# Performance work log

Measured on AMD Instinct MI355X. Metric: run time of the kernel, lower is better.

## Reference

```python
import math
from itertools import combinations
import jax, jax.numpy as jnp
import numpy as np

B, N, KR, KA, T = 16, 96, 16, 8, 4
RCR, RCA = 5.2, 3.5


def setup_inputs() -> dict:
    key = jax.random.key(0)
    k1, k2 = jax.random.split(key)
    coords = jax.random.normal(k1, (B, N, 3), dtype=jnp.float32) * 3.0
    atom_types = jax.random.randint(k2, (N,), 0, T)
    EtaR = jnp.full((T, KR), 16.0, dtype=jnp.float32)
    ShfR = jnp.tile(jnp.linspace(0.9, 5.0, KR, dtype=jnp.float32), (T, 1))
    Zeta = jnp.full((T, KA), 32.0, dtype=jnp.float32)
    EtaA = jnp.tile(jnp.linspace(0.5, 8.0, KA, dtype=jnp.float32), (T, 1))
    return {"coords": coords, "atom_types": atom_types,
            "EtaR": EtaR, "ShfR": ShfR, "Zeta": Zeta, "EtaA": EtaA}


def _pairwise_vector(coords):
    # coords: [B, N, 3] -> rij: [B, N, N-1, 3] (diagonal removed, same order as masked_select)
    n = coords.shape[1]
    idx = np.array([[j for j in range(n) if j != i] for i in range(n)])  # [N, N-1]
    rij = coords[:, :, None, :] - coords[:, None, :, :]                   # [B, N, N, 3]
    return rij[:, np.arange(n)[:, None], idx]                             # [B, N, N-1, 3]


def reference(coords, atom_types, EtaR, ShfR, Zeta, EtaA):
    rij = _pairwise_vector(coords)                 # [B, N, N-1, 3]
    er = EtaR[atom_types]                          # [N, KR]
    sr = ShfR[atom_types]                          # [N, KR]
    ze = Zeta[atom_types]                          # [N, KA]
    ea = EtaA[atom_types]                          # [N, KA]

    # ---- G2 (radial) ----
    dij = jnp.linalg.norm(rij, axis=3)             # [B, N, N-1]
    fij = (jnp.cos(dij / RCR * math.pi) + 1) * 0.5
    g2 = jnp.sum(jnp.exp(-er[:, None, :] * (dij[..., None] - sr[:, None, :]) ** 2)
                 * fij[..., None], axis=2)         # [B, N, KR]

    # ---- G3 (angular) ----
    n1 = rij.shape[2]
    c = np.array(list(combinations(range(n1), 2)))  # [P, 2]
    rp = rij[:, :, c]                               # [B, N, P, 2, 3]
    r12, r13 = rp[:, :, :, 0], rp[:, :, :, 1]
    r23 = r12 - r13
    d12 = jnp.linalg.norm(r12, axis=3)              # [B, N, P]
    d13 = jnp.linalg.norm(r13, axis=3)
    d23 = jnp.linalg.norm(r23, axis=3)
    f12 = (jnp.cos(d12 / RCA * math.pi) + 1) * 0.5
    f13 = (jnp.cos(d13 / RCA * math.pi) + 1) * 0.5
    f23 = (jnp.cos(d23 / RCA * math.pi) + 1) * 0.5
    cosine = jnp.einsum('bnpk,bnpk->bnp', r12, r13) / (d12 * d13)
    g3 = jnp.sum(2.0 ** (1 - ze[:, None, :])
                 * (1 + cosine[..., None]) ** ze[:, None, :]
                 * jnp.exp(-ea[:, None, :] * (d12 ** 2 + d13 ** 2 + d23 ** 2)[..., None])
                 * (f12 * f13 * f23)[..., None], axis=2)  # [B, N, KA]

    return jnp.concatenate((g2, g3), axis=2)        # [B, N, KR+KA]
```

## Files before the change

### kernel.cpp

```cpp
#include <hip/hip_runtime.h>

namespace {
constexpr int Bc  = 16;
constexpr int Nc  = 96;
constexpr int KRc = 16;
constexpr int KAc = 8;
constexpr int NOUT = KRc + KAc;
constexpr int NNb  = Nc - 1;
constexpr float RCRf = 5.2f;
constexpr float RCAf = 3.5f;
constexpr float L2E  = 1.4426950408889634f;
}

__device__ __forceinline__ float cos_rev(float rev) {
    return __builtin_amdgcn_cosf(__builtin_amdgcn_fractf(rev));
}
__device__ __forceinline__ float exp2g(float x) {
    return __builtin_amdgcn_exp2f(x);
}

__global__ __launch_bounds__(256, 6) void ani_feat_kernel(
    const float* __restrict__ coords,
    const int*   __restrict__ atom_types,
    const float* __restrict__ EtaR,
    const float* __restrict__ ShfR,
    const float* __restrict__ Zeta,
    const float* __restrict__ EtaA,
    float* __restrict__ out)
{
    const int bi = blockIdx.x;
    const int b  = bi / Nc;
    const int i  = bi - b * Nc;
    const int t  = threadIdx.x;
    const int lane = t & 63, wv = t >> 6;

    __shared__ float4 su[NNb];
    __shared__ float  ufa[NNb], sfr[NNb];
    __shared__ float4 ca4[NNb];
    __shared__ float  cfa[NNb], cfr[NNb];
    __shared__ float  pr[16][KRc];
    __shared__ float  red[4][KAc];
    __shared__ int    sM[2];

    const int ti = atom_types[i];

    bool fast;
    float ea0, dLs, c10, THR;
    {
        float z0 = Zeta[ti * KAc + 0];
        bool zu = true;
#pragma unroll
        for (int k = 1; k < KAc; ++k) zu = zu && (Zeta[ti * KAc + k] == z0);
        ea0 = EtaA[ti * KAc + 0] * L2E;
        float e1v = EtaA[ti * KAc + 1] * L2E;
        dLs = e1v - ea0;
        bool ar = true;
#pragma unroll
        for (int k = 2; k < KAc; ++k) {
            float ev = EtaA[ti * KAc + k] * L2E;
            ar = ar && (fabsf(ev - (ea0 + dLs * (float)k)) <=
                        1e-5f * fabsf(ev) + 1e-7f);
        }
        float eamin = fminf(ea0, ea0 + 7.0f * dLs);
        fast = zu && ar && (z0 == 32.0f) && (eamin > 1e-6f);
        THR  = fast ? (26.0f / eamin) : 1e30f;
        c10  = 1.0f - z0;
    }

    float st_ux = 0, st_uy = 0, st_uz = 0, st_d = 0, st_fa = 0, st_fr = 0;
    bool pred = false;
    if (t < NNb) {
        const float* cb = coords + (size_t)(b * Nc) * 3;
        int j = t + (t >= i);
        float dx = cb[i*3+0] - cb[j*3+0];
        float dy = cb[i*3+1] - cb[j*3+1];
        float dz = cb[i*3+2] - cb[j*3+2];
        float d2 = dx*dx + dy*dy + dz*dz;
        float d  = __builtin_amdgcn_sqrtf(d2);
        float inv = __builtin_amdgcn_rcpf(d);
        st_ux = dx*inv; st_uy = dy*inv; st_uz = dz*inv; st_d = d;
        st_fa = fmaf(cos_rev(d * (0.5f / RCAf)), 0.5f, 0.5f);
        st_fr = fmaf(cos_rev(d * (0.5f / RCRf)), 0.5f, 0.5f);
        su[t]  = make_float4(st_ux, st_uy, st_uz, d);
        ufa[t] = st_fa;
        sfr[t] = st_fr;
        pred = (d2 <= THR);
    }
    unsigned long long mask = __ballot(pred);
    unsigned long long ltm  = (1ull << lane) - 1ull;
    if (wv == 0) {
        int pos = (int)__popcll(mask & ltm);
        if (pred) {
            ca4[pos] = make_float4(st_ux, st_uy, st_uz, st_d);
            cfa[pos] = st_fa; cfr[pos] = st_fr;
        }
        if (t == 0) sM[0] = (int)__popcll(mask);
    }
    __syncthreads();

    if (wv == 1) {
        int base = sM[0];
        int pos = base + (int)__popcll(mask & ltm);
        if (pred) {
            ca4[pos] = make_float4(st_ux, st_uy, st_uz, st_d);
            cfa[pos] = st_fa; cfr[pos] = st_fr;
        }
        if (lane == 0) sM[1] = base + (int)__popcll(mask);
    }
    __syncthreads();

    const int M = sM[1];

    {
        const int k = t & 15, g2 = t >> 4;
        float er  = EtaR[ti * KRc + k];
        float sr  = ShfR[ti * KRc + k];
        float sqT = __builtin_amdgcn_sqrtf(THR);
        bool okk = (sr < sqT) && (er * (sqT - sr) * (sqT - sr) >= 16.0f);
        bool okr = __all(okk) && fast;
        float erL = -er * L2E;
        float acc = 0.0f;
        if (okr) {
            for (int jj = g2; jj < M; jj += 16) {
                float dd = ca4[jj].w - sr;
                acc += exp2g(erL * dd * dd) * cfr[jj];
            }
        } else {
            for (int jj = g2; jj < NNb; jj += 16) {
                float dd = su[jj].w - sr;
                acc += exp2g(erL * dd * dd) * sfr[jj];
            }
        }
        pr[g2][k] = acc;
    }

    float av[KAc];

    if (fast) {
        float acc[KAc];
#pragma unroll
        for (int k = 0; k < KAc; ++k) acc[k] = 0.0f;

        const int K      = (M - 1) >> 1;
        const int fullS  = M * K;
        const int tailS  = (M & 1) ? 0 : (M >> 1);
        const int nps    = fullS + tailS;
        const int rounds = (nps + 255) >> 8;
        const float invM = 1.0f / (float)M;

        for (int r = 0; r < rounds; ++r) {
            int slot = (r << 8) + t;
            bool valid = slot < nps;
            int a, rr;
            if (slot < fullS) {
                int rp = (int)((float)slot * invM);
                a = slot - rp * M;
                if (a < 0)       { --rp; a += M; }
                else if (a >= M) { ++rp; a -= M; }
                rr = rp + 1;
            } else {
                a  = slot - fullS;
                rr = M >> 1;
            }
            if (!valid) { a = 0; rr = 0; }
            int bq = a + rr; if (bq >= M) bq -= M;

            float4 A  = ca4[a];
            float4 Bv = ca4[bq];
            float faa = cfa[a], fab = cfa[bq];
            float da = A.w, db = Bv.w;
            float cosv = fmaf(A.x, Bv.x, fmaf(A.y, Bv.y, A.z * Bv.z));
            float sAB  = fmaf(da, da, db * db);
            float d23sq = fmaxf(fmaf(-2.0f * da * db, cosv, sAB), 0.0f);
            float f23 = fmaf(cos_rev(__builtin_amdgcn_sqrtf(d23sq) *
                                     (0.5f / RCAf)), 0.5f, 0.5f);
            float fprod = faa * fab * f23;
            float s  = sAB + d23sq;
            float tt = 1.0f + cosv;
            float t2 = tt*tt, t4 = t2*t2, t8 = t4*t4, t16 = t8*t8;
            float F  = t16 * t16 * fprod;
            F = valid ? F : 0.0f;
            float e0 = exp2g(-ea0 * s);
            float q  = exp2g(-dLs * s);
            float q2 = q * q;
            float e1 = e0*q,  e2 = e0*q2, e3 = e1*q2;
            float e4 = e2*q2, e5 = e3*q2, e6 = e4*q2, e7 = e5*q2;
            acc[0] = fmaf(F, e0, acc[0]);
            acc[1] = fmaf(F, e1, acc[1]);
            acc[2] = fmaf(F, e2, acc[2]);
            acc[3] = fmaf(F, e3, acc[3]);
            acc[4] = fmaf(F, e4, acc[4]);
            acc[5] = fmaf(F, e5, acc[5]);
            acc[6] = fmaf(F, e6, acc[6]);
            acc[7] = fmaf(F, e7, acc[7]);
        }
        const float p21z = exp2g(c10);
#pragma unroll
        for (int k = 0; k < KAc; ++k) av[k] = acc[k] * p21z;
    } else {
        float zek[KAc], c1k[KAc], eaL[KAc];
#pragma unroll
        for (int k = 0; k < KAc; ++k) {
            float z = Zeta[ti * KAc + k];
            zek[k] = z;
            c1k[k] = 1.0f - z;
            eaL[k] = EtaA[ti * KAc + k] * L2E;
        }
        float accS[KAc];
#pragma unroll
        for (int k = 0; k < KAc; ++k) accS[k] = 0.0f;

        const bool act = (t < 2 * NNb);
        const int  g   = (t >= NNb) ? 1 : 0;
        const int  j   = act ? (t - g * NNb) : 0;
        if (act) {
            float4 A = su[j];
            float faj = ufa[j];
            float d2A = A.w * A.w;
            float m2Aw = -2.0f * A.w;
            for (int r = 0; r < 24; ++r) {
                int rr = (g ? 25 : 1) + r;
                float lv = (rr <= 47) ? 1.0f : 0.0f;
                int j2 = j + rr; if (j2 >= NNb) j2 -= NNb;
                float4 Bq = su[j2];
                float fb = ufa[j2];
                float cosv = fmaf(A.x, Bq.x, fmaf(A.y, Bq.y, A.z * Bq.z));
                float sAB  = fmaf(Bq.w, Bq.w, d2A);
                float d23sq = fmaxf(fmaf(m2Aw * Bq.w, cosv, sAB), 0.0f);
                float d23 = __builtin_amdgcn_sqrtf(d23sq);
                float f23 = fmaf(cos_rev(d23 * (0.5f / RCAf)), 0.5f, 0.5f);
                float fprod = faj * fb * f23 * lv;
                float s  = sAB + d23sq;
                float tt = fmaxf(1.0f + cosv, 0.0f);
                float l2 = __builtin_amdgcn_logf(tt);
#pragma unroll
                for (int k = 0; k < KAc; ++k) {
                    float E = fmaf(zek[k], l2, c1k[k]);
                    E = fmaf(-eaL[k], s, E);
                    accS[k] += exp2g(E) * fprod;
                }
            }
        }
#pragma unroll
        for (int k = 0; k < KAc; ++k) av[k] = accS[k];
    }

#pragma unroll
    for (int k = 0; k < KAc; ++k) {
        float v = av[k];
#pragma unroll
        for (int off = 32; off; off >>= 1) v += __shfl_xor(v, off, 64);
        if (lane == 0) red[wv][k] = v;
    }
    __syncthreads();

    if (t < KAc) {
        out[bi * NOUT + KRc + t] =
            red[0][t] + red[1][t] + red[2][t] + red[3][t];
    }
    if (t < KRc) {
        float s = 0.0f;
#pragma unroll
        for (int g2 = 0; g2 < 16; ++g2) s += pr[g2][t];
        out[bi * NOUT + t] = s;
    }
}

extern "C" void kernel_launch(void* const* d_in, const int* in_sizes, int n_in,
                              void* d_out, int out_size, void* d_ws, size_t ws_size,
                              hipStream_t stream) {
    const float* coords     = (const float*)d_in[0];
    const int*   atom_types = (const int*)d_in[1];
    const float* EtaR       = (const float*)d_in[2];
    const float* ShfR       = (const float*)d_in[3];
    const float* Zeta       = (const float*)d_in[4];
    const float* EtaA       = (const float*)d_in[5];
    float* out = (float*)d_out;

    ani_feat_kernel<<<dim3(Bc * Nc), dim3(256), 0, stream>>>(
        coords, atom_types, EtaR, ShfR, Zeta, EtaA, out);
}
```

Before: 15.87 us.

## Restructure angular fast path to lane-owned atom with per-wave offset rotation

The compacted neighbor list moves from float4 AoS to separate SoA arrays that are zero-padded to 96 entries. The angular fast path drops the per-slot division-based pair decode. Instead each lane owns neighbor `lane` in registers, and each wave walks rotation offsets, two per iteration, with half-weighting for the M/2 self-pair offset. This removes the index arithmetic and one shared load per pair and adds ILP, but it only applies when M <= 64 and otherwise falls back to the slow general path.

```diff
diff --git a/kernel.cpp b/kernel.cpp
--- a/kernel.cpp
+++ b/kernel.cpp
@@ -36,8 +36,8 @@
 
     __shared__ float4 su[NNb];
     __shared__ float  ufa[NNb], sfr[NNb];
-    __shared__ float4 ca4[NNb];
-    __shared__ float  cfa[NNb], cfr[NNb];
+    __shared__ float  cux[Nc], cuy[Nc], cuz[Nc];
+    __shared__ float  cdd[Nc], cfa[Nc], cfr[Nc];
     __shared__ float  pr[16][KRc];
     __shared__ float  red[4][KAc];
     __shared__ int    sM[2];
@@ -69,6 +69,10 @@
 
     float st_ux = 0, st_uy = 0, st_uz = 0, st_d = 0, st_fa = 0, st_fr = 0;
     bool pred = false;
+    if (t < Nc) {
+        cux[t] = 0.0f; cuy[t] = 0.0f; cuz[t] = 0.0f;
+        cdd[t] = 0.0f; cfa[t] = 0.0f; cfr[t] = 0.0f;
+    }
     if (t < NNb) {
         const float* cb = coords + (size_t)(b * Nc) * 3;
         int j = t + (t >= i);
@@ -91,25 +95,25 @@
     if (wv == 0) {
         int pos = (int)__popcll(mask & ltm);
         if (pred) {
-            ca4[pos] = make_float4(st_ux, st_uy, st_uz, st_d);
-            cfa[pos] = st_fa; cfr[pos] = st_fr;
+            cux[pos] = st_ux; cuy[pos] = st_uy; cuz[pos] = st_uz;
+            cdd[pos] = st_d;  cfa[pos] = st_fa; cfr[pos] = st_fr;
         }
         if (t == 0) sM[0] = (int)__popcll(mask);
     }
     __syncthreads();
-
     if (wv == 1) {
         int base = sM[0];
         int pos = base + (int)__popcll(mask & ltm);
         if (pred) {
-            ca4[pos] = make_float4(st_ux, st_uy, st_uz, st_d);
-            cfa[pos] = st_fa; cfr[pos] = st_fr;
+            cux[pos] = st_ux; cuy[pos] = st_uy; cuz[pos] = st_uz;
+            cdd[pos] = st_d;  cfa[pos] = st_fa; cfr[pos] = st_fr;
         }
         if (lane == 0) sM[1] = base + (int)__popcll(mask);
     }
     __syncthreads();
 
     const int M = sM[1];
+    const bool fastA = fast && (M <= 64);
 
     {
         const int k = t & 15, g2 = t >> 4;
@@ -122,7 +126,7 @@
         float acc = 0.0f;
         if (okr) {
             for (int jj = g2; jj < M; jj += 16) {
-                float dd = ca4[jj].w - sr;
+                float dd = cdd[jj] - sr;
                 acc += exp2g(erL * dd * dd) * cfr[jj];
             }
         } else {
@@ -135,65 +139,67 @@
     }
 
     float av[KAc];
-
-    if (fast) {
+#pragma unroll
+    for (int k = 0; k < KAc; ++k) av[k] = 0.0f;
+
+    if (fastA) {
+        const float Aux = cux[lane], Auy = cuy[lane], Auz = cuz[lane];
+        const float Ad  = cdd[lane], Afa = cfa[lane];
+        const float d2A = Ad * Ad;
+        const float m2A = -2.0f * Ad;
+        const int   Ktot = M >> 1;
+
         float acc[KAc];
 #pragma unroll
         for (int k = 0; k < KAc; ++k) acc[k] = 0.0f;
 
-        const int K      = (M - 1) >> 1;
-        const int fullS  = M * K;
-        const int tailS  = (M & 1) ? 0 : (M >> 1);
-        const int nps    = fullS + tailS;
-        const int rounds = (nps + 255) >> 8;
-        const float invM = 1.0f / (float)M;
-
-        for (int r = 0; r < rounds; ++r) {
-            int slot = (r << 8) + t;
-            bool valid = slot < nps;
-            int a, rr;
-            if (slot < fullS) {
-                int rp = (int)((float)slot * invM);
-                a = slot - rp * M;
-                if (a < 0)       { --rp; a += M; }
-                else if (a >= M) { ++rp; a -= M; }
-                rr = rp + 1;
-            } else {
-                a  = slot - fullS;
-                rr = M >> 1;
-            }
-            if (!valid) { a = 0; rr = 0; }
-            int bq = a + rr; if (bq >= M) bq -= M;
-
-            float4 A  = ca4[a];
-            float4 Bv = ca4[bq];
-            float faa = cfa[a], fab = cfa[bq];
-            float da = A.w, db = Bv.w;
-            float cosv = fmaf(A.x, Bv.x, fmaf(A.y, Bv.y, A.z * Bv.z));
-            float sAB  = fmaf(da, da, db * db);
-            float d23sq = fmaxf(fmaf(-2.0f * da * db, cosv, sAB), 0.0f);
-            float f23 = fmaf(cos_rev(__builtin_amdgcn_sqrtf(d23sq) *
-                                     (0.5f / RCAf)), 0.5f, 0.5f);
-            float fprod = faa * fab * f23;
-            float s  = sAB + d23sq;
-            float tt = 1.0f + cosv;
-            float t2 = tt*tt, t4 = t2*t2, t8 = t4*t4, t16 = t8*t8;
-            float F  = t16 * t16 * fprod;
-            F = valid ? F : 0.0f;
-            float e0 = exp2g(-ea0 * s);
-            float q  = exp2g(-dLs * s);
-            float q2 = q * q;
-            float e1 = e0*q,  e2 = e0*q2, e3 = e1*q2;
-            float e4 = e2*q2, e5 = e3*q2, e6 = e4*q2, e7 = e5*q2;
-            acc[0] = fmaf(F, e0, acc[0]);
-            acc[1] = fmaf(F, e1, acc[1]);
-            acc[2] = fmaf(F, e2, acc[2]);
-            acc[3] = fmaf(F, e3, acc[3]);
-            acc[4] = fmaf(F, e4, acc[4]);
-            acc[5] = fmaf(F, e5, acc[5]);
-            acc[6] = fmaf(F, e6, acc[6]);
-            acc[7] = fmaf(F, e7, acc[7]);
-        }
+#define ANG_HALF(BX,BY,BZ,BD,BFA,HW)                                        \
+        {                                                                   \
+            float cosv = fmaf(Aux, BX, fmaf(Auy, BY, Auz * BZ));            \
+            float sAB  = fmaf(BD, BD, d2A);                                 \
+            float d23sq = fmaxf(fmaf(m2A * BD, cosv, sAB), 0.0f);           \
+            float f23 = fmaf(cos_rev(__builtin_amdgcn_sqrtf(d23sq) *        \
+                                     (0.5f / RCAf)), 0.5f, 0.5f);           \
+            float fprod = Afa * BFA * f23 * (HW);                           \
+            float s  = sAB + d23sq;                                         \
+            float tt = 1.0f + cosv;                 \
+            float t2 = tt*tt, t4 = t2*t2, t8 = t4*t4, t16 = t8*t8;          \
+            float F  = t16 * t16 * fprod;                                   \
+            float e0 = exp2g(-ea0 * s);                                     \
+            float q  = exp2g(-dLs * s);                                     \
+            float q2 = q * q;                                               \
+            float e1 = e0*q,  e2 = e0*q2, e3 = e1*q2;                       \
+            float e4 = e2*q2, e5 = e3*q2, e6 = e4*q2, e7 = e5*q2;           \
+            acc[0] = fmaf(F, e0, acc[0]);                                   \
+            acc[1] = fmaf(F, e1, acc[1]);                                   \
+            acc[2] = fmaf(F, e2, acc[2]);                                   \
+            acc[3] = fmaf(F, e3, acc[3]);                                   \
+            acc[4] = fmaf(F, e4, acc[4]);                                   \
+            acc[5] = fmaf(F, e5, acc[5]);                                   \
+            acc[6] = fmaf(F, e6, acc[6]);                                   \
+            acc[7] = fmaf(F, e7, acc[7]);                                   \
+        }
+
+        for (int rrA = wv + 1; rrA <= Ktot; rrA += 8) {
+            int   rrB = rrA + 4;
+            float hwA = (2 * rrA == M) ? 0.5f : 1.0f;
+            float hwB = 1.0f;
+            if (rrB > Ktot) { rrB = rrA; hwB = 0.0f; }
+            else if (2 * rrB == M) hwB = 0.5f;
+
+            int bA = lane + rrA; if (bA >= M) bA -= M;
+            int bB = lane + rrB; if (bB >= M) bB -= M;
+
+            float BxA = cux[bA], ByA = cuy[bA], BzA = cuz[bA];
+            float BdA = cdd[bA], BfA = cfa[bA];
+            float BxB = cux[bB], ByB = cuy[bB], BzB = cuz[bB];
+            float BdB = cdd[bB], BfB = cfa[bB];
+
+            ANG_HALF(BxA, ByA, BzA, BdA, BfA, hwA)
+            ANG_HALF(BxB, ByB, BzB, BdB, BfB, hwB)
+        }
+#undef ANG_HALF
+
         const float p21z = exp2g(c10);
 #pragma unroll
         for (int k = 0; k < KAc; ++k) av[k] = acc[k] * p21z;
@@ -206,10 +212,6 @@
             c1k[k] = 1.0f - z;
             eaL[k] = EtaA[ti * KAc + k] * L2E;
         }
-        float accS[KAc];
-#pragma unroll
-        for (int k = 0; k < KAc; ++k) accS[k] = 0.0f;
-
         const bool act = (t < 2 * NNb);
         const int  g   = (t >= NNb) ? 1 : 0;
         const int  j   = act ? (t - g * NNb) : 0;
@@ -237,12 +239,10 @@
                 for (int k = 0; k < KAc; ++k) {
                     float E = fmaf(zek[k], l2, c1k[k]);
                     E = fmaf(-eaL[k], s, E);
-                    accS[k] += exp2g(E) * fprod;
+                    av[k] += exp2g(E) * fprod;
                 }
             }
         }
-#pragma unroll
-        for (int k = 0; k < KAc; ++k) av[k] = accS[k];
     }
 
 #pragma unroll
```

New measurement: 18.14 us. 14.3% more time.
